# Kernel optimization log

Hardware: AMD Instinct MI355X
Metric: run time of the kernel (lower is better)

Reference implementation:

```python
import jax, jax.numpy as jnp
import numpy as np


def positional_encoding(max_len, embed_dim):
    pos = jnp.arange(max_len, dtype=jnp.float32)[:, None]          # (L, 1)
    i = jnp.arange(embed_dim, dtype=jnp.float32)[None, :]          # (1, C)
    angle = pos / jnp.power(10000.0, 2.0 * jnp.floor(i / 2.0) / embed_dim)
    pe = jnp.where((jnp.arange(embed_dim) % 2) == 0, jnp.sin(angle), jnp.cos(angle))
    return pe[None, :, :]                                          # (1, L, C)


def setup_inputs() -> dict:
    key = jax.random.key(0)
    k1, k2 = jax.random.split(key)
    x = jax.random.normal(k1, (4, 256, 64, 64), dtype=jnp.float32)
    W_qkv = jax.random.normal(k2, (256, 768), dtype=jnp.float32) * 0.02
    return {"x": x, "W_qkv": W_qkv}


def reference(x, W_qkv):
    N, C, H, W = x.shape
    L = H * W
    num_heads = 8
    head_dim = C // num_heads

    # (N, C, H, W) -> (N, L, C), add sinusoidal positional encoding
    xt = x.reshape(N, C, L).transpose(0, 2, 1) + positional_encoding(L, C)

    # qkv projection (no bias): (N, L, 3C)
    qkv = xt @ W_qkv
    qkv = qkv.reshape(N, L, 3, num_heads, head_dim).transpose(2, 0, 3, 1, 4)
    q, k, v = qkv[0], qkv[1], qkv[2]                               # (N, h, L, d)

    scale = 1.0 / np.sqrt(head_dim).astype(np.float32)
    scores = jnp.einsum('nhqd,nhkd->nhqk', q, k) * scale           # (N, h, L, L)
    attn = jax.nn.softmax(scores, axis=-1)
    out = jnp.einsum('nhqk,nhkd->nhqd', attn, v)                   # (N, h, L, d)

    # (N, h, L, d) -> (N, L, C) -> (N, C, H, W)
    out = out.transpose(0, 2, 1, 3).reshape(N, L, C)
    return out.transpose(0, 2, 1).reshape(N, C, H, W)
```

## Files before the change

### kernel.cpp

```cpp
#include <hip/hip_runtime.h>
#include <hip/hip_bf16.h>

#define L_SEQ 4096
#define C_DIM 256
#define QKV_N 768

typedef short bf16x8 __attribute__((ext_vector_type(8)));
typedef float f32x4  __attribute__((ext_vector_type(4)));
typedef float f32x16 __attribute__((ext_vector_type(16)));

#if defined(__has_builtin)
#  if __has_builtin(__builtin_amdgcn_permlane32_swap)
#    define HAVE_PLSWAP 1
#  endif
#endif

__device__ inline short f2bf(float f){ union{__hip_bfloat16 h; short s;}u; u.h=__float2bfloat16(f); return u.s; }
__device__ inline float bf2f(short s){ union{unsigned u; float f;}x; x.u=((unsigned)(unsigned short)s)<<16; return x.f; }

__device__ inline unsigned cvtpk(float lo, float hi){
  unsigned r;
  asm("v_cvt_pk_bf16_f32 %0, %1, %2" : "=v"(r) : "v"(lo), "v"(hi));
  return r;
}

__device__ inline void plswap(unsigned &a, unsigned &b){
#ifdef HAVE_PLSWAP
  auto r = __builtin_amdgcn_permlane32_swap(a, b, false, false);
  a = r[0]; b = r[1];
#else
  unsigned ax = __shfl_xor((int)a, 32);
  unsigned bx = __shfl_xor((int)b, 32);
  bool hi = (threadIdx.x & 32) != 0;
  unsigned na = hi ? bx : a;
  unsigned nb = hi ? b : ax;
  a = na; b = nb;
#endif
}

__global__ __launch_bounds__(256) void tables_kernel(
    const float* __restrict__ W, short* __restrict__ pe_t, short* __restrict__ wT){
  int bid = blockIdx.x;
  if (bid < 4096){
    int idx = bid*256 + threadIdx.x;
    int c = idx >> 12, l = idx & 4095;
    int c2 = c & ~1;
    float inv = __expf(-(float)c2 * (9.210340371976184f/256.0f));
    float rev = (float)l * inv * 0.15915494309189535f;
    float fr = rev - floorf(rev);
    float v = (c & 1) ? __builtin_amdgcn_cosf(fr) : __builtin_amdgcn_sinf(fr);
    pe_t[idx] = f2bf(v);
  } else {
    int idx = (bid - 4096)*256 + threadIdx.x;
    int jj = idx >> 8, k = idx & 255;
    wT[idx] = f2bf(W[k*QKV_N + jj]);
  }
}

__global__ __launch_bounds__(256) void qkv_gemm(
    const float* __restrict__ x, const short* __restrict__ pe_t, const short* __restrict__ wT,
    short* __restrict__ qw, short* __restrict__ kw, short* __restrict__ vtw){
  __shared__ __align__(16) short A_lds[64][264];
  __shared__ __align__(16) short B_lds[2][192][40];
  int m0 = blockIdx.x * 64;
  int n = m0 >> 12, l0 = m0 & 4095;
  int j0 = blockIdx.y * 192;
  int tid = threadIdx.x;

  {
    int c = tid;
    const float* xp = x + ((size_t)n*C_DIM + c)*L_SEQ + l0;
    const short* pp = pe_t + (size_t)c*L_SEQ + l0;
    float xv[64];
#pragma unroll
    for (int q = 0; q < 16; ++q) *(float4*)&xv[q*4] = ((const float4*)xp)[q];
    short pv[64];
#pragma unroll
    for (int q = 0; q < 8; ++q) *(bf16x8*)&pv[q*8] = ((const bf16x8*)pp)[q];
#pragma unroll
    for (int i = 0; i < 64; ++i) A_lds[i][c] = f2bf(xv[i] + bf2f(pv[i]));
  }
  {
#pragma unroll
    for (int s = 0; s < 3; ++s){
      int chunk = tid + s*256;
      int j = chunk >> 2, kc = chunk & 3;
      *(bf16x8*)&B_lds[0][j][kc*8] = *(const bf16x8*)(wT + (size_t)(j0 + j)*256 + kc*8);
    }
  }
  __syncthreads();

  int wv = tid >> 6, lane = tid & 63, r = lane & 15, g = lane >> 4;
  f32x4 acc[4][3] = {};

  for (int ks = 0; ks < 8; ++ks){
    int buf = ks & 1;
    bf16x8 pre[3];
    if (ks < 7){
#pragma unroll
      for (int s = 0; s < 3; ++s){
        int chunk = tid + s*256;
        int j = chunk >> 2, kc = chunk & 3;
        pre[s] = *(const bf16x8*)(wT + (size_t)(j0 + j)*256 + (ks+1)*32 + kc*8);
      }
    }
    bf16x8 a[4];
#pragma unroll
    for (int mf = 0; mf < 4; ++mf)
      a[mf] = *(const bf16x8*)&A_lds[mf*16 + r][ks*32 + g*8];
#pragma unroll
    for (int t = 0; t < 3; ++t){
      bf16x8 b = *(const bf16x8*)&B_lds[buf][wv*48 + t*16 + r][g*8];
#pragma unroll
      for (int mf = 0; mf < 4; ++mf)
        acc[mf][t] = __builtin_amdgcn_mfma_f32_16x16x32_bf16(a[mf], b, acc[mf][t], 0,0,0);
    }
    if (ks < 7){
#pragma unroll
      for (int s = 0; s < 3; ++s){
        int chunk = tid + s*256;
        int j = chunk >> 2, kc = chunk & 3;
        *(bf16x8*)&B_lds[buf^1][j][kc*8] = pre[s];
      }
    }
    __syncthreads();
  }

  const float QSCALE = 0.17677669529663687f * 1.4426950408889634f;
#pragma unroll
  for (int mf = 0; mf < 4; ++mf)
#pragma unroll
  for (int t = 0; t < 3; ++t)
#pragma unroll
  for (int i = 0; i < 4; ++i){
    int l = l0 + mf*16 + g*4 + i;
    int j = j0 + wv*48 + t*16 + r;
    int which = j >> 8, h = (j >> 5) & 7, d = j & 31;
    int pair = n*8 + h;
    float v = acc[mf][t][i];
    if (which == 0)      qw[((size_t)pair*L_SEQ + l)*32 + d] = f2bf(v * QSCALE);
    else if (which == 1) kw[((size_t)pair*L_SEQ + l)*32 + d] = f2bf(v);
    else                 vtw[((size_t)pair*32 + d)*L_SEQ + l] = f2bf(v);
  }
}

__global__ __launch_bounds__(256,4) void attn_kernel(
    const short* __restrict__ qw, const short* __restrict__ kw,
    const short* __restrict__ vtw, float* __restrict__ out){
  __shared__ __align__(16) short K_lds[2][64][64];
  __shared__ __align__(16) short V_lds[2][32][64];
  const int KB = 64*64*2, VB = 32*64*2;

  int bid = blockIdx.x;
  int xcd = bid & 7, jj = bid >> 3;
  int pair = (jj >> 5)*8 + xcd;
  int q0 = (jj & 31)*128;
  int n = pair >> 3, h = pair & 7;
  int tid = threadIdx.x, wv = tid >> 6, lane = tid & 63;
  int qc = lane & 31, hi = lane >> 5;

  const short* qb_ = qw + (size_t)pair*L_SEQ*32;
  const short* kptr[2]; const short* vptr[2];
  char* kdst[2]; char* vdst[2];
#pragma unroll
  for (int s = 0; s < 2; ++s){
    int idx = tid + s*256;
    int skey = idx >> 3, sdc = idx & 7;
    int svd  = idx >> 4, svc = idx & 15;
    kptr[s] = kw + (size_t)pair*L_SEQ*32 + (size_t)skey*32 + sdc*4;
    vptr[s] = vtw + (size_t)pair*32*L_SEQ + (size_t)svd*L_SEQ + svc*4;
    kdst[s] = (char*)&K_lds[0][skey][0] + (((sdc>>1) ^ (skey&7))*16) + (sdc&1)*8;
    vdst[s] = (char*)&V_lds[0][svd][0] + (((svc>>1) ^ (svd&7))*16) + (svc&1)*8;
  }

  bf16x8 qf0 = *(const bf16x8*)(qb_ + (size_t)(q0 + wv*32 + qc)*32 + hi*8);
  bf16x8 qf1 = *(const bf16x8*)(qb_ + (size_t)(q0 + wv*32 + qc)*32 + 16 + hi*8);

  int ka_off[2][2];
#pragma unroll
  for (int sub = 0; sub < 2; ++sub)
#pragma unroll
  for (int dh = 0; dh < 2; ++dh){
    int row = sub*32 + qc;
    ka_off[sub][dh] = row*128 + (((dh*2 + hi) ^ (row & 7))*16);
  }
  int va_off[4];
#pragma unroll
  for (int m = 0; m < 4; ++m) va_off[m] = qc*128 + (((2*m + hi) ^ (qc & 7))*16);

  const bf16x8 onesv = {0x3F80,0x3F80,0x3F80,0x3F80,0x3F80,0x3F80,0x3F80,0x3F80};

  f32x16 o = {}, ls = {};

  {
#pragma unroll
    for (int s = 0; s < 2; ++s){
      *(int2*)kdst[s] = *(const int2*)kptr[s];
      *(int2*)vdst[s] = *(const int2*)vptr[s];
    }
  }
  __syncthreads();

  for (int t = 0; t < 64; ++t){
    int buf = t & 1;
    const char* kB_ = (const char*)K_lds + buf*KB;
    const char* vB_ = (const char*)V_lds + buf*VB;

    bf16x8 ka00 = *(const bf16x8*)(kB_ + ka_off[0][0]);
    bf16x8 ka01 = *(const bf16x8*)(kB_ + ka_off[0][1]);
    bf16x8 ka10 = *(const bf16x8*)(kB_ + ka_off[1][0]);
    bf16x8 ka11 = *(const bf16x8*)(kB_ + ka_off[1][1]);

    f32x16 z = {};
    __builtin_amdgcn_s_setprio(1);
    f32x16 s0 = __builtin_amdgcn_mfma_f32_32x32x16_bf16(ka00, qf0, z, 0,0,0);
    s0        = __builtin_amdgcn_mfma_f32_32x32x16_bf16(ka01, qf1, s0, 0,0,0);
    f32x16 s1 = __builtin_amdgcn_mfma_f32_32x32x16_bf16(ka10, qf0, z, 0,0,0);
    s1        = __builtin_amdgcn_mfma_f32_32x32x16_bf16(ka11, qf1, s1, 0,0,0);
    __builtin_amdgcn_s_setprio(0);

    int2 kv[2], vv[2];
    bool pf = (t < 63);
    if (pf){
#pragma unroll
      for (int s = 0; s < 2; ++s){
        kptr[s] += 64*32; vptr[s] += 64;
        kv[s] = *(const int2*)kptr[s];
        vv[s] = *(const int2*)vptr[s];
      }
    }

#pragma unroll
    for (int i = 0; i < 16; ++i) s0[i] = __builtin_amdgcn_exp2f(s0[i]);
#pragma unroll
    for (int i = 0; i < 16; ++i) s1[i] = __builtin_amdgcn_exp2f(s1[i]);

#pragma unroll
    for (int m = 0; m < 4; ++m){
      int b = (m & 1)*8;
      unsigned g0a, g0b, g4a, g4b;
      if (m < 2){
        g0a = cvtpk(s0[b+0], s0[b+1]); g0b = cvtpk(s0[b+2], s0[b+3]);
        g4a = cvtpk(s0[b+4], s0[b+5]); g4b = cvtpk(s0[b+6], s0[b+7]);
      } else {
        g0a = cvtpk(s1[b+0], s1[b+1]); g0b = cvtpk(s1[b+2], s1[b+3]);
        g4a = cvtpk(s1[b+4], s1[b+5]); g4b = cvtpk(s1[b+6], s1[b+7]);
      }
      plswap(g0a, g4a);
      plswap(g0b, g4b);
      union{ unsigned w[4]; bf16x8 v; } pu;
      pu.w[0] = g0a; pu.w[1] = g0b; pu.w[2] = g4a; pu.w[3] = g4b;
      bf16x8 va = *(const bf16x8*)(vB_ + va_off[m]);
      o  = __builtin_amdgcn_mfma_f32_32x32x16_bf16(va,    pu.v, o,  0,0,0);
      ls = __builtin_amdgcn_mfma_f32_32x32x16_bf16(onesv, pu.v, ls, 0,0,0);
    }

    if (pf){
#pragma unroll
      for (int s = 0; s < 2; ++s){
        *(int2*)(kdst[s] + (buf^1)*KB) = kv[s];
        *(int2*)(vdst[s] + (buf^1)*VB) = vv[s];
      }
    }
    __syncthreads();
  }

  float rinv = 1.0f / ls[0];
#pragma unroll
  for (int reg = 0; reg < 16; ++reg){
    int d = (reg & 3) + 8*(reg >> 2) + 4*hi;
    out[(size_t)(n*C_DIM + h*32 + d)*L_SEQ + q0 + wv*32 + qc] = o[reg]*rinv;
  }
}

extern "C" void kernel_launch(void* const* d_in, const int* in_sizes, int n_in,
                              void* d_out, int out_size, void* d_ws, size_t ws_size,
                              hipStream_t stream) {
  const float* x = (const float*)d_in[0];
  const float* W = (const float*)d_in[1];
  float* out = (float*)d_out;
  char* ws = (char*)d_ws;
  short* pe_t = (short*)ws;
  short* wT   = (short*)(ws + (size_t)2*1024*1024);
  short* qw   = (short*)(ws + (size_t)3*1024*1024);
  short* kw   = (short*)(ws + (size_t)11*1024*1024);
  short* vtw  = (short*)(ws + (size_t)19*1024*1024);

  tables_kernel<<<dim3(4864), 256, 0, stream>>>(W, pe_t, wT);
  qkv_gemm<<<dim3(256, 4), 256, 0, stream>>>(x, pe_t, wT, qw, kw, vtw);
  attn_kernel<<<dim3(1024), 256, 0, stream>>>(qw, kw, vtw, out);
}
```

Measured before the change: 195.4 us.

## Process two 32-query tiles per wave in attention to reuse K/V fragments

Each wave now handles 64 queries (two 32-row Q tiles) instead of 32, so each block covers 256 queries and the grid halves to 512 blocks. The K and V fragments read from LDS and the global K/V tile loads are shared across twice as many queries, which cuts LDS traffic and global K/V reads per unit of work. In exchange, register pressure roughly doubles for scores and accumulators, launch bounds drop to 2 blocks per SM, and there are fewer blocks to spread across CUs.

```diff
diff --git a/kernel.cpp b/kernel.cpp
--- a/kernel.cpp
+++ b/kernel.cpp
@@ -144,7 +144,7 @@
   }
 }
 
-__global__ __launch_bounds__(256,4) void attn_kernel(
+__global__ __launch_bounds__(256,2) void attn_kernel(
     const short* __restrict__ qw, const short* __restrict__ kw,
     const short* __restrict__ vtw, float* __restrict__ out){
   __shared__ __align__(16) short K_lds[2][64][64];
@@ -153,8 +153,8 @@
 
   int bid = blockIdx.x;
   int xcd = bid & 7, jj = bid >> 3;
-  int pair = (jj >> 5)*8 + xcd;
-  int q0 = (jj & 31)*128;
+  int pair = (jj >> 4)*8 + xcd;
+  int q0 = (jj & 15)*256;
   int n = pair >> 3, h = pair & 7;
   int tid = threadIdx.x, wv = tid >> 6, lane = tid & 63;
   int qc = lane & 31, hi = lane >> 5;
@@ -173,8 +173,12 @@
     vdst[s] = (char*)&V_lds[0][svd][0] + (((svc>>1) ^ (svd&7))*16) + (svc&1)*8;
   }
 
-  bf16x8 qf0 = *(const bf16x8*)(qb_ + (size_t)(q0 + wv*32 + qc)*32 + hi*8);
-  bf16x8 qf1 = *(const bf16x8*)(qb_ + (size_t)(q0 + wv*32 + qc)*32 + 16 + hi*8);
+  const short* qpA = qb_ + (size_t)(q0 + wv*64 +  0 + qc)*32;
+  const short* qpB = qb_ + (size_t)(q0 + wv*64 + 32 + qc)*32;
+  bf16x8 qfA0 = *(const bf16x8*)(qpA + hi*8);
+  bf16x8 qfA1 = *(const bf16x8*)(qpA + 16 + hi*8);
+  bf16x8 qfB0 = *(const bf16x8*)(qpB + hi*8);
+  bf16x8 qfB1 = *(const bf16x8*)(qpB + 16 + hi*8);
 
   int ka_off[2][2];
 #pragma unroll
@@ -190,7 +194,7 @@
 
   const bf16x8 onesv = {0x3F80,0x3F80,0x3F80,0x3F80,0x3F80,0x3F80,0x3F80,0x3F80};
 
-  f32x16 o = {}, ls = {};
+  f32x16 oA = {}, oB = {}, lsA = {}, lsB = {};
 
   {
 #pragma unroll
@@ -213,10 +217,14 @@
 
     f32x16 z = {};
     __builtin_amdgcn_s_setprio(1);
-    f32x16 s0 = __builtin_amdgcn_mfma_f32_32x32x16_bf16(ka00, qf0, z, 0,0,0);
-    s0        = __builtin_amdgcn_mfma_f32_32x32x16_bf16(ka01, qf1, s0, 0,0,0);
-    f32x16 s1 = __builtin_amdgcn_mfma_f32_32x32x16_bf16(ka10, qf0, z, 0,0,0);
-    s1        = __builtin_amdgcn_mfma_f32_32x32x16_bf16(ka11, qf1, s1, 0,0,0);
+    f32x16 sA0 = __builtin_amdgcn_mfma_f32_32x32x16_bf16(ka00, qfA0, z,   0,0,0);
+    sA0        = __builtin_amdgcn_mfma_f32_32x32x16_bf16(ka01, qfA1, sA0, 0,0,0);
+    f32x16 sA1 = __builtin_amdgcn_mfma_f32_32x32x16_bf16(ka10, qfA0, z,   0,0,0);
+    sA1        = __builtin_amdgcn_mfma_f32_32x32x16_bf16(ka11, qfA1, sA1, 0,0,0);
+    f32x16 sB0 = __builtin_amdgcn_mfma_f32_32x32x16_bf16(ka00, qfB0, z,   0,0,0);
+    sB0        = __builtin_amdgcn_mfma_f32_32x32x16_bf16(ka01, qfB1, sB0, 0,0,0);
+    f32x16 sB1 = __builtin_amdgcn_mfma_f32_32x32x16_bf16(ka10, qfB0, z,   0,0,0);
+    sB1        = __builtin_amdgcn_mfma_f32_32x32x16_bf16(ka11, qfB1, sB1, 0,0,0);
     __builtin_amdgcn_s_setprio(0);
 
     int2 kv[2], vv[2];
@@ -231,28 +239,50 @@
     }
 
 #pragma unroll
-    for (int i = 0; i < 16; ++i) s0[i] = __builtin_amdgcn_exp2f(s0[i]);
-#pragma unroll
-    for (int i = 0; i < 16; ++i) s1[i] = __builtin_amdgcn_exp2f(s1[i]);
+    for (int i = 0; i < 16; ++i) sA0[i] = __builtin_amdgcn_exp2f(sA0[i]);
+#pragma unroll
+    for (int i = 0; i < 16; ++i) sA1[i] = __builtin_amdgcn_exp2f(sA1[i]);
+#pragma unroll
+    for (int i = 0; i < 16; ++i) sB0[i] = __builtin_amdgcn_exp2f(sB0[i]);
+#pragma unroll
+    for (int i = 0; i < 16; ++i) sB1[i] = __builtin_amdgcn_exp2f(sB1[i]);
 
 #pragma unroll
     for (int m = 0; m < 4; ++m){
       int b = (m & 1)*8;
-      unsigned g0a, g0b, g4a, g4b;
-      if (m < 2){
-        g0a = cvtpk(s0[b+0], s0[b+1]); g0b = cvtpk(s0[b+2], s0[b+3]);
-        g4a = cvtpk(s0[b+4], s0[b+5]); g4b = cvtpk(s0[b+6], s0[b+7]);
-      } else {
-        g0a = cvtpk(s1[b+0], s1[b+1]); g0b = cvtpk(s1[b+2], s1[b+3]);
-        g4a = cvtpk(s1[b+4], s1[b+5]); g4b = cvtpk(s1[b+6], s1[b+7]);
-      }
-      plswap(g0a, g4a);
-      plswap(g0b, g4b);
-      union{ unsigned w[4]; bf16x8 v; } pu;
-      pu.w[0] = g0a; pu.w[1] = g0b; pu.w[2] = g4a; pu.w[3] = g4b;
       bf16x8 va = *(const bf16x8*)(vB_ + va_off[m]);
-      o  = __builtin_amdgcn_mfma_f32_32x32x16_bf16(va,    pu.v, o,  0,0,0);
-      ls = __builtin_amdgcn_mfma_f32_32x32x16_bf16(onesv, pu.v, ls, 0,0,0);
+      {
+        unsigned g0a, g0b, g4a, g4b;
+        if (m < 2){
+          g0a = cvtpk(sA0[b+0], sA0[b+1]); g0b = cvtpk(sA0[b+2], sA0[b+3]);
+          g4a = cvtpk(sA0[b+4], sA0[b+5]); g4b = cvtpk(sA0[b+6], sA0[b+7]);
+        } else {
+          g0a = cvtpk(sA1[b+0], sA1[b+1]); g0b = cvtpk(sA1[b+2], sA1[b+3]);
+          g4a = cvtpk(sA1[b+4], sA1[b+5]); g4b = cvtpk(sA1[b+6], sA1[b+7]);
+        }
+        plswap(g0a, g4a);
+        plswap(g0b, g4b);
+        union{ unsigned w[4]; bf16x8 v; } pu;
+        pu.w[0] = g0a; pu.w[1] = g0b; pu.w[2] = g4a; pu.w[3] = g4b;
+        oA  = __builtin_amdgcn_mfma_f32_32x32x16_bf16(va,    pu.v, oA,  0,0,0);
+        lsA = __builtin_amdgcn_mfma_f32_32x32x16_bf16(onesv, pu.v, lsA, 0,0,0);
+      }
+      {
+        unsigned g0a, g0b, g4a, g4b;
+        if (m < 2){
+          g0a = cvtpk(sB0[b+0], sB0[b+1]); g0b = cvtpk(sB0[b+2], sB0[b+3]);
+          g4a = cvtpk(sB0[b+4], sB0[b+5]); g4b = cvtpk(sB0[b+6], sB0[b+7]);
+        } else {
+          g0a = cvtpk(sB1[b+0], sB1[b+1]); g0b = cvtpk(sB1[b+2], sB1[b+3]);
+          g4a = cvtpk(sB1[b+4], sB1[b+5]); g4b = cvtpk(sB1[b+6], sB1[b+7]);
+        }
+        plswap(g0a, g4a);
+        plswap(g0b, g4b);
+        union{ unsigned w[4]; bf16x8 v; } pu;
+        pu.w[0] = g0a; pu.w[1] = g0b; pu.w[2] = g4a; pu.w[3] = g4b;
+        oB  = __builtin_amdgcn_mfma_f32_32x32x16_bf16(va,    pu.v, oB,  0,0,0);
+        lsB = __builtin_amdgcn_mfma_f32_32x32x16_bf16(onesv, pu.v, lsB, 0,0,0);
+      }
     }
 
     if (pf){
@@ -265,11 +295,14 @@
     __syncthreads();
   }
 
-  float rinv = 1.0f / ls[0];
+  float rinvA = 1.0f / lsA[0];
+  float rinvB = 1.0f / lsB[0];
 #pragma unroll
   for (int reg = 0; reg < 16; ++reg){
     int d = (reg & 3) + 8*(reg >> 2) + 4*hi;
-    out[(size_t)(n*C_DIM + h*32 + d)*L_SEQ + q0 + wv*32 + qc] = o[reg]*rinv;
+    size_t base = (size_t)(n*C_DIM + h*32 + d)*L_SEQ + q0 + wv*64 + qc;
+    out[base]      = oA[reg]*rinvA;
+    out[base + 32] = oB[reg]*rinvB;
   }
 }
 
@@ -288,5 +321,5 @@
 
   tables_kernel<<<dim3(4864), 256, 0, stream>>>(W, pe_t, wT);
   qkv_gemm<<<dim3(256, 4), 256, 0, stream>>>(x, pe_t, wT, qw, kw, vtw);
-  attn_kernel<<<dim3(1024), 256, 0, stream>>>(qw, kw, vtw, out);
-}
+  attn_kernel<<<dim3(512), 256, 0, stream>>>(qw, kw, vtw, out);
+}
```

Result: faster. 185.5 us (-5.1%).
